# Performance work log

Measured on AMD Instinct MI355X. Metric: run time of the kernel, lower is better.

The kernel has to match this reference:

```python
import jax, jax.numpy as jnp
import numpy as np

B, T, C, H, NT = 1, 1024, 768, 12, 8
D = C // H  # 64
POWER_ITERS = 4
DP_TEMP = 0.8
ESR_GAMMA = 0.02
ESR_ALPHA = 0.1


def rmsnorm(x, w, eps=1e-6):
    rms = jax.lax.rsqrt(jnp.mean(x * x, axis=-1, keepdims=True) + eps)
    return x * rms * w


def setup_inputs():
    key = jax.random.key(0)
    k0, k1, k2 = jax.random.split(key, 3)
    return {
        "x": jax.random.normal(k0, (B, T, C), jnp.float32),
        "W_qkvg": jax.random.normal(k1, (4 * C, C), jnp.float32) * 0.02,
        "W_out": jax.random.normal(k2, (C, C), jnp.float32) * 0.02,
        "lam": jnp.float32(1.5),
        "log_tau": -0.5 * jnp.ones((H, NT), jnp.float32),
        "logit_w": jnp.zeros((H, NT), jnp.float32),
        "beta": 1.5 * jnp.ones((H,), jnp.float32),
        "out_scale": jnp.ones((H,), jnp.float32),
        "dp_scale": jnp.ones((H,), jnp.float32),
        "logk_scale": jnp.ones((H,), jnp.float32),
        "dt_logit": jnp.float32(np.log(1.0 / 1e-8)),  # dt=1.0 -> logit = log(dt/(1-dt+1e-8))
        "g_norm_w": jnp.ones((D,), jnp.float32),
    }


def reference(x, W_qkvg, W_out, lam, log_tau, logit_w, beta, out_scale,
              dp_scale, logk_scale, dt_logit, g_norm_w):
    # qkvg projection and head split
    qkvg = x @ W_qkvg.T                                    # [B,T,4C]
    q, k, v, g = jnp.split(qkvg, 4, axis=-1)
    to_heads = lambda t: t.reshape(B, T, H, D).transpose(0, 2, 1, 3)  # [B,H,T,D]
    q, k, v, g = map(to_heads, (q, k, v, g))
    g = rmsnorm(g, g_norm_w)

    # pairwise squared distance ||g_i - g_j||^2
    g2 = jnp.sum(g * g, axis=-1)                           # [B,H,T]
    s = jnp.maximum(g2[..., :, None] + g2[..., None, :]
                    - 2.0 * jnp.einsum('bhid,bhjd->bhij', g, g), 0.0)  # [B,H,T,T]

    # fractional log-kernel: logsumexp_t[-(beta/2) log1p(s/(4 tau_t)) + log w_t]
    tau = jnp.maximum(jnp.exp(log_tau), 1e-6)              # [H,NT]
    w = jax.nn.softmax(logit_w, axis=-1)                   # [H,NT]
    beta_c = jnp.clip(beta, 0.5, 2.5)                      # [H]
    log_k_per = -(beta_c[None, :, None, None, None] / 2.0) * jnp.log1p(
        s[:, :, None] / (4.0 * tau[None, :, :, None, None]))          # [B,H,NT,T,T]
    logK = jax.nn.logsumexp(log_k_per + jnp.log(w + 1e-12)[None, :, :, None, None], axis=2)
    logK = logK * logk_scale[None, :, None, None]

    # dot-product scores
    dp = jnp.einsum('bhid,bhjd->bhij', q, k) * (dp_scale[None, :, None, None]
                                                / (np.sqrt(D) * DP_TEMP))

    # causal Markov normalize: blend, mask, stable row-softmax
    mask = jnp.tril(jnp.ones((T, T), bool))[None, None]    # [1,1,T,T]
    blended = lam * dp + (1.0 - lam) * logK
    blended = jnp.where(mask, blended, -jnp.inf)
    mx = jnp.max(blended, axis=-1, keepdims=True)
    mx = jnp.where(jnp.isfinite(mx), mx, 0.0)
    Kmat = jnp.exp(jnp.maximum(blended - mx, -60.0)) * mask
    P = Kmat / jnp.maximum(Kmat.sum(-1, keepdims=True), 1e-12)

    # power iteration for left stationary pi with full-support teleport
    pi0 = jnp.full((B, H, 1, T), 1.0 / T, P.dtype)
    def step(pi, _):
        p = (1.0 - ESR_GAMMA) * (pi @ P) + ESR_GAMMA / T
        p = p / jnp.maximum(p.sum(-1, keepdims=True), 1e-12)
        return p, None
    pi, _ = jax.lax.scan(step, pi0, None, length=POWER_ITERS)
    pi = jax.lax.stop_gradient(pi[..., 0, :])              # [B,H,T] (detached)

    # causal approximation to additive reversibilization
    P_adj = (pi[..., None, :] / jnp.maximum(pi[..., :, None], 1e-12)) \
            * jnp.swapaxes(P, -1, -2)                      # P*_ij = (pi_j/pi_i) P_ji
    P_rev = 0.5 * (P + P_adj) * mask
    P_rev = P_rev / jnp.maximum(P_rev.sum(-1, keepdims=True), 1e-12)

    dt = jax.nn.sigmoid(dt_logit)
    alpha = ESR_ALPHA * dt                                  # scale_alpha_by_dt=True
    P_fin = (1.0 - alpha) * P + alpha * P_rev

    y = (P_fin @ v) * out_scale[None, :, None, None]       # [B,H,T,D]
    y = y.transpose(0, 2, 1, 3).reshape(B, T, C)
    return y @ W_out.T
```

## Files before the change

kernel.cpp:

```cpp
#include <hip/hip_runtime.h>
#include <math.h>

#define TSEQ 1024
#define CD   768
#define HN   12
#define DD   64

#define OFF_QH     0
#define OFF_KH     393216
#define OFF_GH     786432
#define OFF_VHT    1179648
#define OFF_VH     1572864
#define OFF_G2     1966080
#define OFF_YB     1978368
#define OFF_CONSTS 2371584
#define OFF_OPART  2372096
#define OFF_LS     8663552
#define OFF_PD     8761856
#define OFF_XB     8774144
#define OFF_WQB    9167360
#define OFF_WOB    10347008

#define NG_X  98304
#define NG_WQ 294912
#define NG_WO 73728

typedef __bf16 bf16x8 __attribute__((ext_vector_type(8)));
typedef float  f32x4  __attribute__((ext_vector_type(4)));
typedef unsigned short u16x8 __attribute__((ext_vector_type(8)));
typedef unsigned short u16x4 __attribute__((ext_vector_type(4)));

__device__ inline unsigned short f2bf(float f) {
  unsigned int u = __float_as_uint(f);
  return (unsigned short)((u + 0x7fffu + ((u >> 16) & 1u)) >> 16);
}
__device__ inline float bf2f(unsigned short u) {
  return __uint_as_float((unsigned)u << 16);
}


__global__ __launch_bounds__(64) void prep_kernel(
    const float* __restrict__ lam_p, const float* __restrict__ log_tau,
    const float* __restrict__ logit_w, const float* __restrict__ beta,
    const float* __restrict__ out_scale, const float* __restrict__ dp_scale,
    const float* __restrict__ logk_scale, const float* __restrict__ dt_logit,
    float* __restrict__ consts) {
  int h = threadIdx.x;
  if (h == 0) {
    float dt = 1.0f / (1.0f + __expf(-dt_logit[0]));
    consts[288] = 0.1f * dt;
  }
  if (h < HN) {
    float lam = lam_p[0];
    float* c = consts + h * 24;
    c[0] = lam * dp_scale[h] * (1.0f / 6.4f);
    c[1] = (1.0f - lam) * logk_scale[h];
    float b = fminf(fmaxf(beta[h], 0.5f), 2.5f);
    c[2] = 0.5f * b;
    c[3] = out_scale[h];
    float m = -1e30f;
    float lw[8];
    bool uni = true;
    for (int t = 0; t < 8; t++) {
      lw[t] = logit_w[h * 8 + t];
      m = fmaxf(m, lw[t]);
      if (log_tau[h * 8 + t] != log_tau[h * 8] || lw[t] != lw[0]) uni = false;
    }
    float s = 0.f;
    float e[8];
    for (int t = 0; t < 8; t++) { e[t] = __expf(lw[t] - m); s += e[t]; }
    for (int t = 0; t < 8; t++) {
      float w = e[t] / s;
      c[12 + t] = log2f(w + 1e-12f);
      float tau = fmaxf(__expf(log_tau[h * 8 + t]), 1e-6f);
      c[4 + t] = 1.0f / (4.0f * tau);
    }
    c[20] = uni ? 1.0f : 8.0f;
  }
}

__global__ __launch_bounds__(256) void convert_kernel(
    const float* __restrict__ x, const float* __restrict__ wq,
    const float* __restrict__ wo, unsigned short* __restrict__ swzA,
    unsigned short* __restrict__ swzWQ, unsigned short* __restrict__ swzWO) {
  int g = blockIdx.x * 256 + threadIdx.x;
  const float* src;
  unsigned short* dst;
  int lg;
  if (g < NG_X) { src = x; dst = swzA; lg = g; }
  else if (g < NG_X + NG_WQ) { src = wq; dst = swzWQ; lg = g - NG_X; }
  else if (g < NG_X + NG_WQ + NG_WO) { src = wo; dst = swzWO; lg = g - NG_X - NG_WQ; }
  else return;
  int lane = lg & 63;
  int kb = (lg >> 6) % 24;
  int t16 = lg / (64 * 24);
  int row = t16 * 16 + (lane & 15);
  int col = kb * 32 + (lane >> 4) * 8;
  const float* s = &src[(size_t)row * 768 + col];
  float4 a = *(const float4*)s;
  float4 b = *(const float4*)(s + 4);
  u16x8 u;
  u[0] = f2bf(a.x); u[1] = f2bf(a.y); u[2] = f2bf(a.z); u[3] = f2bf(a.w);
  u[4] = f2bf(b.x); u[5] = f2bf(b.y); u[6] = f2bf(b.z); u[7] = f2bf(b.w);
  *(u16x8*)&dst[(size_t)lg * 8] = u;
}

__global__ __launch_bounds__(256) void gemm_frag_qkvg(
    const unsigned short* __restrict__ swzA, const unsigned short* __restrict__ swzB,
    const float* __restrict__ consts, const float* __restrict__ g_norm_w,
    unsigned short* __restrict__ qh, unsigned short* __restrict__ kh,
    unsigned short* __restrict__ gh, unsigned short* __restrict__ vh,
    unsigned short* __restrict__ vhT, float* __restrict__ g2) {
  __shared__ __align__(16) unsigned short Ls[128 * 72];
  int t = threadIdx.x, lane = t & 63, w = t >> 6;
  int quad = lane >> 4, tx = lane & 15;
  int ntile = blockIdx.x;
  int m0 = blockIdx.y * 128;
  int nt0 = ntile * 4;
  int mt0 = blockIdx.y * 8 + w * 2;

  f32x4 acc[2][4] = {};
#pragma unroll 2
  for (int kb = 0; kb < 24; kb++) {
    bf16x8 a0 = *(const bf16x8*)&swzA[((size_t)((mt0 + 0) * 24 + kb) * 64 + lane) * 8];
    bf16x8 a1 = *(const bf16x8*)&swzA[((size_t)((mt0 + 1) * 24 + kb) * 64 + lane) * 8];
#pragma unroll
    for (int ni = 0; ni < 4; ni++) {
      bf16x8 b = *(const bf16x8*)&swzB[((size_t)((nt0 + ni) * 24 + kb) * 64 + lane) * 8];
      acc[0][ni] = __builtin_amdgcn_mfma_f32_16x16x32_bf16(a0, b, acc[0][ni], 0, 0, 0);
      acc[1][ni] = __builtin_amdgcn_mfma_f32_16x16x32_bf16(a1, b, acc[1][ni], 0, 0, 0);
    }
  }

  int typ = ntile / 12;
  int h = ntile % 12;
  unsigned short* Lw = Ls + w * (32 * 72);
  int mrow0 = m0 + w * 32;

  if (typ == 3) {
    float gw4[4];
#pragma unroll
    for (int ni = 0; ni < 4; ni++) gw4[ni] = g_norm_w[ni * 16 + tx];
#pragma unroll
    for (int mi = 0; mi < 2; mi++) {
#pragma unroll
      for (int reg = 0; reg < 4; reg++) {
        float s1 = acc[mi][0][reg] * acc[mi][0][reg] + acc[mi][1][reg] * acc[mi][1][reg]
                 + acc[mi][2][reg] * acc[mi][2][reg] + acc[mi][3][reg] * acc[mi][3][reg];
#pragma unroll
        for (int m = 1; m < 16; m <<= 1) s1 += __shfl_xor(s1, m, 64);
        float rms = rsqrtf(s1 * (1.f / 64.f) + 1e-6f);
        int rl = mi * 16 + quad * 4 + reg;
        float s2 = 0.f;
#pragma unroll
        for (int ni = 0; ni < 4; ni++) {
          float v = acc[mi][ni][reg] * rms * gw4[ni];
          unsigned short us = f2bf(v);
          Lw[rl * 72 + ni * 16 + tx] = us;
          float vb = bf2f(us);
          s2 += vb * vb;
        }
#pragma unroll
        for (int m = 1; m < 16; m <<= 1) s2 += __shfl_xor(s2, m, 64);
        if (tx == 0) g2[h * 1024 + mrow0 + rl] = s2;
      }
    }
#pragma unroll
    for (int rep = 0; rep < 4; rep++) {
      int idx = rep * 64 + lane;
      int r = idx >> 3, cc = (idx & 7) * 8;
      *(u16x8*)&gh[(size_t)(h * 1024 + mrow0 + r) * 64 + cc] = *(const u16x8*)&Lw[r * 72 + cc];
    }
  } else {
    float sc = (typ == 0) ? consts[h * 24] * 1.44269504089f : 1.0f;
#pragma unroll
    for (int mi = 0; mi < 2; mi++)
#pragma unroll
      for (int ni = 0; ni < 4; ni++)
#pragma unroll
        for (int reg = 0; reg < 4; reg++) {
          int rl = mi * 16 + quad * 4 + reg;
          Lw[rl * 72 + ni * 16 + tx] = f2bf(acc[mi][ni][reg] * sc);
        }
    unsigned short* dst = (typ == 0) ? qh : ((typ == 1) ? kh : vh);
#pragma unroll
    for (int rep = 0; rep < 4; rep++) {
      int idx = rep * 64 + lane;
      int r = idx >> 3, cc = (idx & 7) * 8;
      *(u16x8*)&dst[(size_t)(h * 1024 + mrow0 + r) * 64 + cc] = *(const u16x8*)&Lw[r * 72 + cc];
    }
    if (typ == 2) {
#pragma unroll
      for (int rep = 0; rep < 4; rep++) {
        int idx = rep * 64 + lane;
        int d = idx >> 2, rc = (idx & 3) * 8;
        u16x8 u;
#pragma unroll
        for (int j = 0; j < 8; j++) u[j] = Lw[(rc + j) * 72 + d];
        *(u16x8*)&vhT[(size_t)(h * 64 + d) * 1024 + mrow0 + rc] = u;
      }
    }
  }
}

__global__ __launch_bounds__(256) void gemm_frag_out(
    const unsigned short* __restrict__ swzA, const unsigned short* __restrict__ swzB,
    float* __restrict__ Cm) {
  int t = threadIdx.x, lane = t & 63, w = t >> 6;
  int quad = lane >> 4, tx = lane & 15;
  int n0 = blockIdx.x * 64;
  int m0 = blockIdx.y * 128;
  int nt0 = blockIdx.x * 4;
  int mt0 = blockIdx.y * 8 + w * 2;

  f32x4 acc[2][4] = {};
#pragma unroll 2
  for (int kb = 0; kb < 24; kb++) {
    bf16x8 a0 = *(const bf16x8*)&swzA[((size_t)((mt0 + 0) * 24 + kb) * 64 + lane) * 8];
    bf16x8 a1 = *(const bf16x8*)&swzA[((size_t)((mt0 + 1) * 24 + kb) * 64 + lane) * 8];
#pragma unroll
    for (int ni = 0; ni < 4; ni++) {
      bf16x8 b = *(const bf16x8*)&swzB[((size_t)((nt0 + ni) * 24 + kb) * 64 + lane) * 8];
      acc[0][ni] = __builtin_amdgcn_mfma_f32_16x16x32_bf16(a0, b, acc[0][ni], 0, 0, 0);
      acc[1][ni] = __builtin_amdgcn_mfma_f32_16x16x32_bf16(a1, b, acc[1][ni], 0, 0, 0);
    }
  }
#pragma unroll
  for (int mi = 0; mi < 2; mi++)
#pragma unroll
    for (int ni = 0; ni < 4; ni++)
#pragma unroll
      for (int reg = 0; reg < 4; reg++) {
        int row = m0 + w * 32 + mi * 16 + quad * 4 + reg;
        Cm[(size_t)row * CD + n0 + ni * 16 + tx] = acc[mi][ni][reg];
      }
}

__global__ __launch_bounds__(256, 3) void flash_kernel(
    const unsigned short* __restrict__ qh, const unsigned short* __restrict__ kh,
    const unsigned short* __restrict__ gh, const unsigned short* __restrict__ vhT,
    const float* __restrict__ g2, const float* __restrict__ consts,
    float* __restrict__ Opart, float* __restrict__ lsp, float* __restrict__ pdp) {
  int h = blockIdx.y;
  int uu = 143 - (int)blockIdx.x;
  int it = 0, rem = uu;
  for (it = 0; it < 32; ++it) {
    int njt_ = (it >> 1) + 1;
    int nc = (njt_ + 1) >> 1;
    if (rem < nc) break;
    rem -= nc;
  }
  int njt = (it >> 1) + 1;
  int jt0 = rem * 2;
  int jt1 = (jt0 + 2 < njt) ? (jt0 + 2) : njt;
  bool owns_diag = (jt1 == njt);
  int i0 = it * 32;
  int t = threadIdx.x;
  int lane = t & 63, w = t >> 6;
  int quad = lane >> 4, tx = lane & 15;
  int mi = w >> 1, nb = (w & 1) * 2;

  __shared__ __align__(16) unsigned short Qa[32 * 72];
  __shared__ __align__(16) unsigned short Ga[32 * 72];
  __shared__ __align__(16) unsigned short Ks[64 * 72];
  __shared__ __align__(16) unsigned short Gjs[64 * 72];
  __shared__ __align__(16) unsigned short Vt[64 * 72];
  __shared__ __align__(16) unsigned short psh[32 * 72];
  __shared__ float g2i[32], g2j[64], pdiag[32], lsum[32];

  const float* ch = consts + h * 24;
  float lkc = ch[1], bh2 = ch[2];
  int ntt = (int)ch[20];
  float i4t0 = ch[4];
  float inv4tau[8], logw[8];
#pragma unroll
  for (int tt = 0; tt < 8; tt++) { inv4tau[tt] = ch[4 + tt]; logw[tt] = ch[12 + tt]; }

  {
    int r = t >> 3, c8 = (t & 7) * 8;
    *(u16x8*)&Qa[r * 72 + c8] = *(const u16x8*)&qh[(size_t)(h * 1024 + i0 + r) * 64 + c8];
    *(u16x8*)&Ga[r * 72 + c8] = *(const u16x8*)&gh[(size_t)(h * 1024 + i0 + r) * 64 + c8];
  }
  if (t < 32) { g2i[t] = g2[h * 1024 + i0 + t]; pdiag[t] = 0.f; }
  __syncthreads();

  bf16x8 aq[2], ag[2];
#pragma unroll
  for (int ks = 0; ks < 2; ks++) {
    aq[ks] = *(const bf16x8*)&Qa[(mi * 16 + tx) * 72 + ks * 32 + quad * 8];
    ag[ks] = *(const bf16x8*)&Ga[(mi * 16 + tx) * 72 + ks * 32 + quad * 8];
  }

  f32x4 Oc[2] = {};
  float rowacc[4] = {0.f, 0.f, 0.f, 0.f};
  int r4 = t >> 2, cb = (t & 3) * 16;

  for (int jt = jt0; jt < jt1; jt++) {
    int j0 = jt * 64;
    __syncthreads();
    {
      const unsigned short* kp = &kh[(size_t)(h * 1024 + j0 + r4) * 64 + cb];
      const unsigned short* gp = &gh[(size_t)(h * 1024 + j0 + r4) * 64 + cb];
      const unsigned short* vp = &vhT[(size_t)(h * 64 + r4) * 1024 + j0 + cb];
      *(u16x8*)&Ks[r4 * 72 + cb] = *(const u16x8*)kp;
      *(u16x8*)&Ks[r4 * 72 + cb + 8] = *(const u16x8*)(kp + 8);
      *(u16x8*)&Gjs[r4 * 72 + cb] = *(const u16x8*)gp;
      *(u16x8*)&Gjs[r4 * 72 + cb + 8] = *(const u16x8*)(gp + 8);
      *(u16x8*)&Vt[r4 * 72 + cb] = *(const u16x8*)vp;
      *(u16x8*)&Vt[r4 * 72 + cb + 8] = *(const u16x8*)(vp + 8);
    }
    if (t < 64) g2j[t] = g2[h * 1024 + j0 + t];
    __syncthreads();

    f32x4 sqk[2] = {}, sgg[2] = {};
#pragma unroll
    for (int ni2 = 0; ni2 < 2; ni2++) {
#pragma unroll
      for (int ks = 0; ks < 2; ks++) {
        bf16x8 bk = *(const bf16x8*)&Ks[((nb + ni2) * 16 + tx) * 72 + ks * 32 + quad * 8];
        sqk[ni2] = __builtin_amdgcn_mfma_f32_16x16x32_bf16(aq[ks], bk, sqk[ni2], 0, 0, 0);
        bf16x8 bg = *(const bf16x8*)&Gjs[((nb + ni2) * 16 + tx) * 72 + ks * 32 + quad * 8];
        sgg[ni2] = __builtin_amdgcn_mfma_f32_16x16x32_bf16(ag[ks], bg, sgg[ni2], 0, 0, 0);
      }
    }

    float rs[4] = {0.f, 0.f, 0.f, 0.f};
#pragma unroll
    for (int ni2 = 0; ni2 < 2; ni2++) {
      int colg = j0 + (nb + ni2) * 16 + tx;
      float g2jv = g2j[(nb + ni2) * 16 + tx];
#pragma unroll
      for (int reg = 0; reg < 4; reg++) {
        int rowl = mi * 16 + quad * 4 + reg;
        int gi = i0 + rowl;
        float s = fmaxf(g2i[rowl] + g2jv - 2.0f * sgg[ni2][reg], 0.0f);
        float lse2;
        if (ntt == 1) {
          lse2 = -bh2 * __builtin_amdgcn_logf(fmaf(s, i4t0, 1.0f));
        } else {
          float se = 0.f;
#pragma unroll
          for (int tt = 0; tt < 8; tt++) {
            float lv = __builtin_amdgcn_logf(fmaf(s, inv4tau[tt], 1.0f));
            se += __builtin_amdgcn_exp2f(fmaf(-bh2, lv, logw[tt]));
          }
          lse2 = __builtin_amdgcn_logf(se + 1e-30f);
        }
        float b = fmaf(lkc, lse2, sqk[ni2][reg]);
        float p = (colg <= gi) ? __builtin_amdgcn_exp2f(b) : 0.0f;
        rs[reg] += p;
        psh[rowl * 72 + (nb + ni2) * 16 + tx] = f2bf(p);
        if (colg == gi) pdiag[rowl] = p;
      }
    }
#pragma unroll
    for (int reg = 0; reg < 4; reg++) {
#pragma unroll
      for (int m = 1; m < 16; m <<= 1) rs[reg] += __shfl_xor(rs[reg], m, 64);
      rowacc[reg] += rs[reg];
    }
    __syncthreads();

    bf16x8 ap[2];
#pragma unroll
    for (int ks = 0; ks < 2; ks++)
      ap[ks] = *(const bf16x8*)&psh[(mi * 16 + tx) * 72 + ks * 32 + quad * 8];
#pragma unroll
    for (int nd2 = 0; nd2 < 2; nd2++) {
#pragma unroll
      for (int ks = 0; ks < 2; ks++) {
        bf16x8 bv = *(const bf16x8*)&Vt[((nb + nd2) * 16 + tx) * 72 + ks * 32 + quad * 8];
        Oc[nd2] = __builtin_amdgcn_mfma_f32_16x16x32_bf16(ap[ks], bv, Oc[nd2], 0, 0, 0);
      }
    }
  }

  if ((w & 1) == 0 && tx == 0) {
#pragma unroll
    for (int reg = 0; reg < 4; reg++) lsum[mi * 16 + quad * 4 + reg] = rowacc[reg];
  }
  __syncthreads();
  if ((w & 1) == 1 && tx == 0) {
#pragma unroll
    for (int reg = 0; reg < 4; reg++) {
      int rowl = mi * 16 + quad * 4 + reg;
      lsp[(size_t)(rem * HN + h) * 1024 + i0 + rowl] = lsum[rowl] + rowacc[reg];
    }
  }
  float* Ob = Opart + (size_t)((rem * HN + h) * 1024 + i0) * 64;
#pragma unroll
  for (int nd2 = 0; nd2 < 2; nd2++) {
#pragma unroll
    for (int reg = 0; reg < 4; reg++) {
      int rowl = mi * 16 + quad * 4 + reg;
      Ob[rowl * 64 + (nb + nd2) * 16 + tx] = Oc[nd2][reg];
    }
  }
  if (owns_diag && t < 32) pdp[h * 1024 + i0 + t] = pdiag[t];
}

__global__ __launch_bounds__(256) void finalize_kernel(
    const float* __restrict__ Opart, const float* __restrict__ lsp,
    const float* __restrict__ pdp, const unsigned short* __restrict__ vh,
    const float* __restrict__ consts, unsigned short* __restrict__ yb) {
  int h = blockIdx.y;
  int t = threadIdx.x;
  int rl = t >> 4, d4 = t & 15;
  int gi = blockIdx.x * 16 + rl;
  int it = gi >> 5;
  int nc = (((it >> 1) + 1) + 1) >> 1;
  float alpha = consts[288];
  float osc = consts[h * 24 + 3];
  float4 Ov = make_float4(0.f, 0.f, 0.f, 0.f);
  float l = 0.f;
  for (int c = 0; c < nc; c++) {
    float4 p = *(const float4*)&Opart[(size_t)((c * HN + h) * 1024 + gi) * 64 + 4 * d4];
    Ov.x += p.x; Ov.y += p.y; Ov.z += p.z; Ov.w += p.w;
    l += lsp[(size_t)(c * HN + h) * 1024 + gi];
  }
  l = fmaxf(l, 1e-12f);
  float Pii = pdp[h * TSEQ + gi] / l;
  float inv1p = 1.0f / (1.0f + Pii);
  float c1 = (1.0f - alpha) + alpha * inv1p;
  float c2 = alpha * Pii * inv1p;
  float invl = 1.0f / l;
  u16x4 vb = *(const u16x4*)&vh[(size_t)(h * 1024 + gi) * 64 + 4 * d4];
  u16x4 o;
  o[0] = f2bf(osc * (c1 * Ov.x * invl + c2 * bf2f(vb[0])));
  o[1] = f2bf(osc * (c1 * Ov.y * invl + c2 * bf2f(vb[1])));
  o[2] = f2bf(osc * (c1 * Ov.z * invl + c2 * bf2f(vb[2])));
  o[3] = f2bf(osc * (c1 * Ov.w * invl + c2 * bf2f(vb[3])));
  int k = h * 64 + 4 * d4;
  int kb = k >> 5, q8 = (k & 31) >> 3, j0 = k & 7;
  int mt = gi >> 4, txl = gi & 15;
  size_t off = (((size_t)mt * 24 + kb) * 64 + q8 * 16 + txl) * 8 + j0;
  *(u16x4*)&yb[off] = o;
}

extern "C" void kernel_launch(void* const* d_in, const int* in_sizes, int n_in,
                              void* d_out, int out_size, void* d_ws, size_t ws_size,
                              hipStream_t stream) {
  (void)in_sizes; (void)n_in; (void)out_size; (void)ws_size;
  const float* x          = (const float*)d_in[0];
  const float* W_qkvg     = (const float*)d_in[1];
  const float* W_out      = (const float*)d_in[2];
  const float* lam        = (const float*)d_in[3];
  const float* log_tau    = (const float*)d_in[4];
  const float* logit_w    = (const float*)d_in[5];
  const float* beta       = (const float*)d_in[6];
  const float* out_scale  = (const float*)d_in[7];
  const float* dp_scale   = (const float*)d_in[8];
  const float* logk_scale = (const float*)d_in[9];
  const float* dt_logit   = (const float*)d_in[10];
  const float* g_norm_w   = (const float*)d_in[11];
  float* ws = (float*)d_ws;
  unsigned short* qh  = (unsigned short*)(ws + OFF_QH);
  unsigned short* kh  = (unsigned short*)(ws + OFF_KH);
  unsigned short* gh  = (unsigned short*)(ws + OFF_GH);
  unsigned short* vhT = (unsigned short*)(ws + OFF_VHT);
  unsigned short* vh  = (unsigned short*)(ws + OFF_VH);
  float* g2     = ws + OFF_G2;
  unsigned short* yb  = (unsigned short*)(ws + OFF_YB);
  float* consts = ws + OFF_CONSTS;
  float* Opart  = ws + OFF_OPART;
  float* lsp    = ws + OFF_LS;
  float* pdp    = ws + OFF_PD;
  unsigned short* swzA = (unsigned short*)(ws + OFF_XB);
  unsigned short* swzWQ = (unsigned short*)(ws + OFF_WQB);
  unsigned short* swzWO = (unsigned short*)(ws + OFF_WOB);
  float* out = (float*)d_out;

  prep_kernel<<<dim3(1), dim3(64), 0, stream>>>(lam, log_tau, logit_w, beta,
                                                out_scale, dp_scale, logk_scale,
                                                dt_logit, consts);
  convert_kernel<<<dim3((NG_X + NG_WQ + NG_WO) / 256), dim3(256), 0, stream>>>(
      x, W_qkvg, W_out, swzA, swzWQ, swzWO);
  gemm_frag_qkvg<<<dim3(48, 8), dim3(256), 0, stream>>>(swzA, swzWQ, consts, g_norm_w,
                                                        qh, kh, gh, vh, vhT, g2);
  flash_kernel<<<dim3(144, 12), dim3(256), 0, stream>>>(qh, kh, gh, vhT, g2, consts,
                                                        Opart, lsp, pdp);
  finalize_kernel<<<dim3(64, 12), dim3(256), 0, stream>>>(Opart, lsp, pdp, vh, consts, yb);
  gemm_frag_out<<<dim3(12, 8), dim3(256), 0, stream>>>(yb, swzWO, out);
}
```

Before: 156.2 us.

## Prefetch K/G/V tiles into registers, widen flash chunks, fold prep into convert

The flash kernel now loads the next key/gate/value tile into registers while the current tile is being computed, which hides global-load latency behind the MFMA work. Each block now covers up to four key tiles instead of two, so there are fewer blocks and fewer partial outputs for finalize to sum. Q/G staging reuses the Ks/Gjs shared buffers to cut LDS use, and launch bounds are raised to allow four blocks per CU. The prep kernel is merged into convert_kernel to save a launch. The costs are more registers for the prefetch and a coarser, less balanced grid.

```diff
diff --git a/kernel.cpp b/kernel.cpp
--- a/kernel.cpp
+++ b/kernel.cpp
@@ -5,6 +5,7 @@
 #define CD   768
 #define HN   12
 #define DD   64
+#define CH   4
 
 #define OFF_QH     0
 #define OFF_KH     393216
@@ -15,11 +16,11 @@
 #define OFF_YB     1978368
 #define OFF_CONSTS 2371584
 #define OFF_OPART  2372096
-#define OFF_LS     8663552
-#define OFF_PD     8761856
-#define OFF_XB     8774144
-#define OFF_WQB    9167360
-#define OFF_WOB    10347008
+#define OFF_LS     5517824
+#define OFF_PD     5566976
+#define OFF_XB     5579264
+#define OFF_WQB    5972480
+#define OFF_WOB    7152128
 
 #define NG_X  98304
 #define NG_WQ 294912
@@ -39,50 +40,49 @@
 }
 
 
-__global__ __launch_bounds__(64) void prep_kernel(
+__global__ __launch_bounds__(256) void convert_kernel(
+    const float* __restrict__ x, const float* __restrict__ wq,
+    const float* __restrict__ wo, unsigned short* __restrict__ swzA,
+    unsigned short* __restrict__ swzWQ, unsigned short* __restrict__ swzWO,
     const float* __restrict__ lam_p, const float* __restrict__ log_tau,
     const float* __restrict__ logit_w, const float* __restrict__ beta,
     const float* __restrict__ out_scale, const float* __restrict__ dp_scale,
     const float* __restrict__ logk_scale, const float* __restrict__ dt_logit,
     float* __restrict__ consts) {
-  int h = threadIdx.x;
-  if (h == 0) {
-    float dt = 1.0f / (1.0f + __expf(-dt_logit[0]));
-    consts[288] = 0.1f * dt;
-  }
-  if (h < HN) {
-    float lam = lam_p[0];
-    float* c = consts + h * 24;
-    c[0] = lam * dp_scale[h] * (1.0f / 6.4f);
-    c[1] = (1.0f - lam) * logk_scale[h];
-    float b = fminf(fmaxf(beta[h], 0.5f), 2.5f);
-    c[2] = 0.5f * b;
-    c[3] = out_scale[h];
-    float m = -1e30f;
-    float lw[8];
-    bool uni = true;
-    for (int t = 0; t < 8; t++) {
-      lw[t] = logit_w[h * 8 + t];
-      m = fmaxf(m, lw[t]);
-      if (log_tau[h * 8 + t] != log_tau[h * 8] || lw[t] != lw[0]) uni = false;
-    }
-    float s = 0.f;
-    float e[8];
-    for (int t = 0; t < 8; t++) { e[t] = __expf(lw[t] - m); s += e[t]; }
-    for (int t = 0; t < 8; t++) {
-      float w = e[t] / s;
-      c[12 + t] = log2f(w + 1e-12f);
-      float tau = fmaxf(__expf(log_tau[h * 8 + t]), 1e-6f);
-      c[4 + t] = 1.0f / (4.0f * tau);
-    }
-    c[20] = uni ? 1.0f : 8.0f;
-  }
-}
-
-__global__ __launch_bounds__(256) void convert_kernel(
-    const float* __restrict__ x, const float* __restrict__ wq,
-    const float* __restrict__ wo, unsigned short* __restrict__ swzA,
-    unsigned short* __restrict__ swzWQ, unsigned short* __restrict__ swzWO) {
+  if (blockIdx.x == 0 && threadIdx.x < 64) {
+    int h = threadIdx.x;
+    if (h == 0) {
+      float dt = 1.0f / (1.0f + __expf(-dt_logit[0]));
+      consts[288] = 0.1f * dt;
+    }
+    if (h < HN) {
+      float lam = lam_p[0];
+      float* c = consts + h * 24;
+      c[0] = lam * dp_scale[h] * (1.0f / 6.4f);
+      c[1] = (1.0f - lam) * logk_scale[h];
+      float b = fminf(fmaxf(beta[h], 0.5f), 2.5f);
+      c[2] = 0.5f * b;
+      c[3] = out_scale[h];
+      float m = -1e30f;
+      float lw[8];
+      bool uni = true;
+      for (int t = 0; t < 8; t++) {
+        lw[t] = logit_w[h * 8 + t];
+        m = fmaxf(m, lw[t]);
+        if (log_tau[h * 8 + t] != log_tau[h * 8] || lw[t] != lw[0]) uni = false;
+      }
+      float s = 0.f;
+      float e[8];
+      for (int t = 0; t < 8; t++) { e[t] = __expf(lw[t] - m); s += e[t]; }
+      for (int t = 0; t < 8; t++) {
+        float w = e[t] / s;
+        c[12 + t] = log2f(w + 1e-12f);
+        float tau = fmaxf(__expf(log_tau[h * 8 + t]), 1e-6f);
+        c[4 + t] = 1.0f / (4.0f * tau);
+      }
+      c[20] = uni ? 1.0f : 8.0f;
+    }
+  }
   int g = blockIdx.x * 256 + threadIdx.x;
   const float* src;
   unsigned short* dst;
@@ -236,23 +236,23 @@
       }
 }
 
-__global__ __launch_bounds__(256, 3) void flash_kernel(
+__global__ __launch_bounds__(256, 4) void flash_kernel(
     const unsigned short* __restrict__ qh, const unsigned short* __restrict__ kh,
     const unsigned short* __restrict__ gh, const unsigned short* __restrict__ vhT,
     const float* __restrict__ g2, const float* __restrict__ consts,
     float* __restrict__ Opart, float* __restrict__ lsp, float* __restrict__ pdp) {
   int h = blockIdx.y;
-  int uu = 143 - (int)blockIdx.x;
+  int uu = 79 - (int)blockIdx.x;
   int it = 0, rem = uu;
   for (it = 0; it < 32; ++it) {
     int njt_ = (it >> 1) + 1;
-    int nc = (njt_ + 1) >> 1;
+    int nc = (njt_ + CH - 1) / CH;
     if (rem < nc) break;
     rem -= nc;
   }
   int njt = (it >> 1) + 1;
-  int jt0 = rem * 2;
-  int jt1 = (jt0 + 2 < njt) ? (jt0 + 2) : njt;
+  int jt0 = rem * CH;
+  int jt1 = (jt0 + CH < njt) ? (jt0 + CH) : njt;
   bool owns_diag = (jt1 == njt);
   int i0 = it * 32;
   int t = threadIdx.x;
@@ -260,8 +260,6 @@
   int quad = lane >> 4, tx = lane & 15;
   int mi = w >> 1, nb = (w & 1) * 2;
 
-  __shared__ __align__(16) unsigned short Qa[32 * 72];
-  __shared__ __align__(16) unsigned short Ga[32 * 72];
   __shared__ __align__(16) unsigned short Ks[64 * 72];
   __shared__ __align__(16) unsigned short Gjs[64 * 72];
   __shared__ __align__(16) unsigned short Vt[64 * 72];
@@ -278,8 +276,8 @@
 
   {
     int r = t >> 3, c8 = (t & 7) * 8;
-    *(u16x8*)&Qa[r * 72 + c8] = *(const u16x8*)&qh[(size_t)(h * 1024 + i0 + r) * 64 + c8];
-    *(u16x8*)&Ga[r * 72 + c8] = *(const u16x8*)&gh[(size_t)(h * 1024 + i0 + r) * 64 + c8];
+    *(u16x8*)&Ks[r * 72 + c8] = *(const u16x8*)&qh[(size_t)(h * 1024 + i0 + r) * 64 + c8];
+    *(u16x8*)&Gjs[r * 72 + c8] = *(const u16x8*)&gh[(size_t)(h * 1024 + i0 + r) * 64 + c8];
   }
   if (t < 32) { g2i[t] = g2[h * 1024 + i0 + t]; pdiag[t] = 0.f; }
   __syncthreads();
@@ -287,30 +285,49 @@
   bf16x8 aq[2], ag[2];
 #pragma unroll
   for (int ks = 0; ks < 2; ks++) {
-    aq[ks] = *(const bf16x8*)&Qa[(mi * 16 + tx) * 72 + ks * 32 + quad * 8];
-    ag[ks] = *(const bf16x8*)&Ga[(mi * 16 + tx) * 72 + ks * 32 + quad * 8];
+    aq[ks] = *(const bf16x8*)&Ks[(mi * 16 + tx) * 72 + ks * 32 + quad * 8];
+    ag[ks] = *(const bf16x8*)&Gjs[(mi * 16 + tx) * 72 + ks * 32 + quad * 8];
   }
 
   f32x4 Oc[2] = {};
   float rowacc[4] = {0.f, 0.f, 0.f, 0.f};
   int r4 = t >> 2, cb = (t & 3) * 16;
 
+  u16x8 pk0, pk1, pg0, pg1, pv0, pv1;
+  float pg2 = 0.f;
+  {
+    int j0 = jt0 * 64;
+    const unsigned short* kp = &kh[(size_t)(h * 1024 + j0 + r4) * 64 + cb];
+    const unsigned short* gp = &gh[(size_t)(h * 1024 + j0 + r4) * 64 + cb];
+    const unsigned short* vp = &vhT[(size_t)(h * 64 + r4) * 1024 + j0 + cb];
+    pk0 = *(const u16x8*)kp; pk1 = *(const u16x8*)(kp + 8);
+    pg0 = *(const u16x8*)gp; pg1 = *(const u16x8*)(gp + 8);
+    pv0 = *(const u16x8*)vp; pv1 = *(const u16x8*)(vp + 8);
+    if (t < 64) pg2 = g2[h * 1024 + j0 + t];
+  }
+
   for (int jt = jt0; jt < jt1; jt++) {
     int j0 = jt * 64;
     __syncthreads();
-    {
-      const unsigned short* kp = &kh[(size_t)(h * 1024 + j0 + r4) * 64 + cb];
-      const unsigned short* gp = &gh[(size_t)(h * 1024 + j0 + r4) * 64 + cb];
-      const unsigned short* vp = &vhT[(size_t)(h * 64 + r4) * 1024 + j0 + cb];
-      *(u16x8*)&Ks[r4 * 72 + cb] = *(const u16x8*)kp;
-      *(u16x8*)&Ks[r4 * 72 + cb + 8] = *(const u16x8*)(kp + 8);
-      *(u16x8*)&Gjs[r4 * 72 + cb] = *(const u16x8*)gp;
-      *(u16x8*)&Gjs[r4 * 72 + cb + 8] = *(const u16x8*)(gp + 8);
-      *(u16x8*)&Vt[r4 * 72 + cb] = *(const u16x8*)vp;
-      *(u16x8*)&Vt[r4 * 72 + cb + 8] = *(const u16x8*)(vp + 8);
-    }
-    if (t < 64) g2j[t] = g2[h * 1024 + j0 + t];
+    *(u16x8*)&Ks[r4 * 72 + cb] = pk0;
+    *(u16x8*)&Ks[r4 * 72 + cb + 8] = pk1;
+    *(u16x8*)&Gjs[r4 * 72 + cb] = pg0;
+    *(u16x8*)&Gjs[r4 * 72 + cb + 8] = pg1;
+    *(u16x8*)&Vt[r4 * 72 + cb] = pv0;
+    *(u16x8*)&Vt[r4 * 72 + cb + 8] = pv1;
+    if (t < 64) g2j[t] = pg2;
     __syncthreads();
+
+    if (jt + 1 < jt1) {
+      int jn = j0 + 64;
+      const unsigned short* kp = &kh[(size_t)(h * 1024 + jn + r4) * 64 + cb];
+      const unsigned short* gp = &gh[(size_t)(h * 1024 + jn + r4) * 64 + cb];
+      const unsigned short* vp = &vhT[(size_t)(h * 64 + r4) * 1024 + jn + cb];
+      pk0 = *(const u16x8*)kp; pk1 = *(const u16x8*)(kp + 8);
+      pg0 = *(const u16x8*)gp; pg1 = *(const u16x8*)(gp + 8);
+      pv0 = *(const u16x8*)vp; pv1 = *(const u16x8*)(vp + 8);
+      if (t < 64) pg2 = g2[h * 1024 + jn + t];
+    }
 
     f32x4 sqk[2] = {}, sgg[2] = {};
 #pragma unroll
@@ -408,7 +425,8 @@
   int rl = t >> 4, d4 = t & 15;
   int gi = blockIdx.x * 16 + rl;
   int it = gi >> 5;
-  int nc = (((it >> 1) + 1) + 1) >> 1;
+  int njt = (it >> 1) + 1;
+  int nc = (njt + CH - 1) / CH;
   float alpha = consts[288];
   float osc = consts[h * 24 + 3];
   float4 Ov = make_float4(0.f, 0.f, 0.f, 0.f);
@@ -470,15 +488,13 @@
   unsigned short* swzWO = (unsigned short*)(ws + OFF_WOB);
   float* out = (float*)d_out;
 
-  prep_kernel<<<dim3(1), dim3(64), 0, stream>>>(lam, log_tau, logit_w, beta,
-                                                out_scale, dp_scale, logk_scale,
-                                                dt_logit, consts);
   convert_kernel<<<dim3((NG_X + NG_WQ + NG_WO) / 256), dim3(256), 0, stream>>>(
-      x, W_qkvg, W_out, swzA, swzWQ, swzWO);
+      x, W_qkvg, W_out, swzA, swzWQ, swzWO,
+      lam, log_tau, logit_w, beta, out_scale, dp_scale, logk_scale, dt_logit, consts);
   gemm_frag_qkvg<<<dim3(48, 8), dim3(256), 0, stream>>>(swzA, swzWQ, consts, g_norm_w,
                                                         qh, kh, gh, vh, vhT, g2);
-  flash_kernel<<<dim3(144, 12), dim3(256), 0, stream>>>(qh, kh, gh, vhT, g2, consts,
-                                                        Opart, lsp, pdp);
+  flash_kernel<<<dim3(80, 12), dim3(256), 0, stream>>>(qh, kh, gh, vhT, g2, consts,
+                                                       Opart, lsp, pdp);
   finalize_kernel<<<dim3(64, 12), dim3(256), 0, stream>>>(Opart, lsp, pdp, vh, consts, yb);
   gemm_frag_out<<<dim3(12, 8), dim3(256), 0, stream>>>(yb, swzWO, out);
 }
```

New measurement: 149.6 us. 4.2% less time.
